# Kernel optimization log

Hardware: AMD Instinct MI355X
Metric: run time of the kernel (lower is better)

Reference implementation:

```python
import jax, jax.numpy as jnp
import numpy as np

LN_EPS = 1e-5
LEAKY_SLOPE = 0.01  # torch nn.LeakyReLU default negative_slope


def layer_norm(x, gamma, beta):
    mu = jnp.mean(x, axis=-1, keepdims=True)
    var = jnp.mean(jnp.square(x - mu), axis=-1, keepdims=True)
    return (x - mu) * jax.lax.rsqrt(var + LN_EPS) * gamma + beta


def setup_inputs() -> dict:
    key = jax.random.key(0)
    k1, k2, k3 = jax.random.split(key, 3)
    B, N, D = 32, 128, 64
    embeddings = jax.random.normal(k1, (B, N, D), dtype=jnp.float32)
    ln_gamma = jnp.ones((D,), dtype=jnp.float32)
    ln_beta = jnp.zeros((D,), dtype=jnp.float32)
    # nn.Linear(3*D, 1): weight [1, 3D], bias [1]
    bound = 1.0 / np.sqrt(3 * D)
    att_w = jax.random.uniform(k2, (1, 3 * D), dtype=jnp.float32, minval=-bound, maxval=bound)
    att_b = jax.random.uniform(k3, (1,), dtype=jnp.float32, minval=-bound, maxval=bound)
    return {"embeddings": embeddings, "ln_gamma": ln_gamma, "ln_beta": ln_beta,
            "att_w": att_w, "att_b": att_b}


def reference(embeddings, ln_gamma, ln_beta, att_w, att_b):
    # embeddings: [B, N, D]
    D = embeddings.shape[-1]
    w = att_w[0]
    w_q, w_k, w_v = w[:D], w[D:2 * D], w[2 * D:]

    # value = query * key (all-pairs elementwise product), [B, N, N, D]
    value = embeddings[:, :, None, :] * embeddings[:, None, :, :]

    # LayerNorm of the broadcast query/key is just a per-node LayerNorm,
    # broadcast N-fold -> compute once per node, then contract with the
    # corresponding slice of the concat-linear weight.
    ln_e = layer_norm(embeddings, ln_gamma, ln_beta)           # [B, N, D]
    q_score = ln_e @ w_q                                        # [B, N]
    k_score = ln_e @ w_k                                        # [B, N]
    v_score = jnp.einsum('bijd,d->bij', layer_norm(value, ln_gamma, ln_beta), w_v)

    # score = Linear(concat(wq, wk, wv)) : [B, N, N]
    score = q_score[:, :, None] + k_score[:, None, :] + v_score + att_b[0]
    score = jnp.where(score >= 0, score, LEAKY_SLOPE * score)   # LeakyReLU
    # dropout is identity in eval mode
    alphas = jax.nn.softmax(score, axis=-1)[..., None]          # [B, N, N, 1]
    return (alphas, value)
```

## Files before the change

### kernel.cpp

```cpp
#include <hip/hip_runtime.h>

#define N_TOK 128
#define DIM   64
#define LN_EPS 1e-5f
#define SLOPE  0.01f

__device__ __forceinline__ float wave_reduce_sum(float v) {
#pragma unroll
    for (int off = 32; off >= 1; off >>= 1) v += __shfl_xor(v, off, 64);
    return v;
}
__device__ __forceinline__ float wave_reduce_max(float v) {
#pragma unroll
    for (int off = 32; off >= 1; off >>= 1) v = fmaxf(v, __shfl_xor(v, off, 64));
    return v;
}

__global__ __launch_bounds__(256) void k0_row_stats(
        const float* __restrict__ emb, const float* __restrict__ gamma,
        const float* __restrict__ beta, const float* __restrict__ attw,
        float* __restrict__ q_ws, float* __restrict__ k_ws, int nrows) {
    int wave = threadIdx.x >> 6, lane = threadIdx.x & 63;
    int r = blockIdx.x * 4 + wave;
    if (r >= nrows) return;
    float e  = emb[r * DIM + lane];
    float g  = gamma[lane], bt = beta[lane];
    float wq = attw[lane], wk = attw[DIM + lane];
    float gwq = g * wq, gwk = g * wk;

    float se  = wave_reduce_sum(e);
    float se2 = wave_reduce_sum(e * e);
    float sq  = wave_reduce_sum(e * gwq);
    float sk  = wave_reduce_sum(e * gwk);
    float Sgq = wave_reduce_sum(gwq);
    float Sbq = wave_reduce_sum(bt * wq);
    float Sgk = wave_reduce_sum(gwk);
    float Sbk = wave_reduce_sum(bt * wk);

    if (lane == 0) {
        float mu  = se * (1.f / 64.f);
        float var = se2 * (1.f / 64.f) - mu * mu;
        float rsq = rsqrtf(var + LN_EPS);
        q_ws[r] = rsq * (sq - mu * Sgq) + Sbq;
        k_ws[r] = rsq * (sk - mu * Sgk) + Sbk;
    }
}

__global__ __launch_bounds__(256) void k1_scores(
        const float* __restrict__ emb, const float* __restrict__ gamma,
        const float* __restrict__ beta, const float* __restrict__ attw,
        const float* __restrict__ attb, const float* __restrict__ q_ws,
        const float* __restrict__ k_ws, float* __restrict__ alphas) {
    __shared__ float e_tr[DIM * N_TOK];
    __shared__ float EV[2][DIM];
    __shared__ float sc_lds[2][N_TOK];
    __shared__ float S[3];

    int b  = blockIdx.x >> 6;
    int i0 = (blockIdx.x & 63) * 2;

    const float4* E4 = (const float4*)(emb + (size_t)b * (N_TOK * DIM));
#pragma unroll
    for (int l = 0; l < 8; ++l) {
        int idx4 = l * 256 + threadIdx.x;
        int j = idx4 >> 4, c = idx4 & 15;
        float4 v = E4[idx4];
        int d0 = c * 4;
        e_tr[(d0 + 0) * N_TOK + (j ^ ((d0 + 0) & 31))] = v.x;
        e_tr[(d0 + 1) * N_TOK + (j ^ ((d0 + 1) & 31))] = v.y;
        e_tr[(d0 + 2) * N_TOK + (j ^ ((d0 + 2) & 31))] = v.z;
        e_tr[(d0 + 3) * N_TOK + (j ^ ((d0 + 3) & 31))] = v.w;
    }
    __syncthreads();

    if (threadIdx.x < 64) {
        int d = threadIdx.x;
        float g = gamma[d], bt = beta[d], wv = attw[2 * DIM + d];
        float sg = wave_reduce_sum(g * wv);
        float sb = wave_reduce_sum(bt * wv);
        if (d == 0) { S[0] = sg; S[1] = sb; S[2] = attb[0]; }
    } else if (threadIdx.x >= 128) {
        int t2 = threadIdx.x - 128;
        int il = t2 >> 6, d = t2 & 63;
        int i = i0 + il;
        float ei = e_tr[d * N_TOK + (i ^ (d & 31))];
        EV[il][d] = ei * gamma[d] * attw[2 * DIM + d];
    }
    __syncthreads();

    int w = threadIdx.x >> 6, lane = threadIdx.x & 63;
    int il = w >> 1, i = i0 + il;
    int j  = ((w & 1) << 6) | lane;
    float qi = q_ws[b * N_TOK + i];
    float kj = k_ws[b * N_TOK + j];
    float s1 = 0.f, s2 = 0.f, s3 = 0.f;
#pragma unroll
    for (int d = 0; d < DIM; ++d) {
        float ej = e_tr[d * N_TOK + (j ^ (d & 31))];
        float pi = e_tr[d * N_TOK + (i ^ (d & 31))];
        float t  = pi * ej;
        s1 += t;
        s2 = fmaf(t, t, s2);
        s3 = fmaf(EV[il][d], ej, s3);
    }
    float mu  = s1 * (1.f / 64.f);
    float var = s2 * (1.f / 64.f) - mu * mu;
    float rsq = rsqrtf(var + LN_EPS);
    float vsc = rsq * (s3 - mu * S[0]) + S[1];
    float sc  = qi + kj + vsc + S[2];
    sc = sc >= 0.f ? sc : SLOPE * sc;
    sc_lds[il][j] = sc;
    __syncthreads();

    if (w < 2) {
        float a  = sc_lds[w][lane];
        float bb = sc_lds[w][lane + 64];
        float m  = wave_reduce_max(fmaxf(a, bb));
        float ea = __expf(a - m), eb = __expf(bb - m);
        float s  = wave_reduce_sum(ea + eb);
        float inv = 1.f / s;
        float* arow = alphas + ((size_t)(b * N_TOK + i0 + w)) * N_TOK;
        arow[lane]      = ea * inv;
        arow[lane + 64] = eb * inv;
    }
}

__global__ __launch_bounds__(256) void k2_value(
        const float* __restrict__ emb, float4* __restrict__ out4, int total4) {
    const float4* E4 = (const float4*)emb;
    int tid = blockIdx.x * 256 + threadIdx.x;
    int stride = gridDim.x * 256;
    for (int idx4 = tid; idx4 < total4; idx4 += stride) {
        int c = idx4 & 15;
        int j = (idx4 >> 4) & 127;
        int i = (idx4 >> 11) & 127;
        int b = idx4 >> 18;
        float4 a = E4[(((b << 7) | i) << 4) | c];
        float4 e = E4[(((b << 7) | j) << 4) | c];
        float4 v;
        v.x = a.x * e.x; v.y = a.y * e.y; v.z = a.z * e.z; v.w = a.w * e.w;
        out4[idx4] = v;
    }
}

extern "C" void kernel_launch(void* const* d_in, const int* in_sizes, int n_in,
                              void* d_out, int out_size, void* d_ws, size_t ws_size,
                              hipStream_t stream) {
    const float* emb   = (const float*)d_in[0];
    const float* gamma = (const float*)d_in[1];
    const float* beta  = (const float*)d_in[2];
    const float* attw  = (const float*)d_in[3];
    const float* attb  = (const float*)d_in[4];
    float* out = (float*)d_out;

    int B = in_sizes[0] / (N_TOK * DIM);
    int nrows = B * N_TOK;
    float* q_ws = (float*)d_ws;
    float* k_ws = q_ws + nrows;

    float* alphas = out;
    float* value  = out + (size_t)nrows * N_TOK;
    int total4 = B * N_TOK * N_TOK * (DIM / 4);

    k0_row_stats<<<dim3((nrows + 3) / 4), dim3(256), 0, stream>>>(
        emb, gamma, beta, attw, q_ws, k_ws, nrows);
    k1_scores<<<dim3(B * 64), dim3(256), 0, stream>>>(
        emb, gamma, beta, attw, attb, q_ws, k_ws, alphas);
    k2_value<<<dim3(B * 128), dim3(256), 0, stream>>>(
        emb, (float4*)value, total4);
}
```

Before: 162.0 us.

## Fuse score computation and value product into one per-row kernel

Merges the score/softmax kernel and the value-writing kernel into one kernel with one block per (batch, query row). Each thread computes a float4 of the elementwise product, writes it to the value output, and reduces LayerNorm statistics across 16-lane groups with shuffles, so the products are computed once instead of twice. This drops the LDS transpose and one launch. In exchange it adds shuffle reductions per element group and rereads the embeddings from global or cache for every row.

```diff
diff --git a/kernel.cpp b/kernel.cpp
--- a/kernel.cpp
+++ b/kernel.cpp
@@ -46,100 +46,78 @@
     }
 }
 
-__global__ __launch_bounds__(256) void k1_scores(
+__global__ __launch_bounds__(256) void k12_fused(
         const float* __restrict__ emb, const float* __restrict__ gamma,
         const float* __restrict__ beta, const float* __restrict__ attw,
         const float* __restrict__ attb, const float* __restrict__ q_ws,
-        const float* __restrict__ k_ws, float* __restrict__ alphas) {
-    __shared__ float e_tr[DIM * N_TOK];
-    __shared__ float EV[2][DIM];
-    __shared__ float sc_lds[2][N_TOK];
-    __shared__ float S[3];
+        const float* __restrict__ k_ws, float* __restrict__ alphas,
+        float4* __restrict__ value4) {
+    __shared__ float sc_lds[N_TOK];
 
-    int b  = blockIdx.x >> 6;
-    int i0 = (blockIdx.x & 63) * 2;
+    int b = blockIdx.x >> 7;
+    int i = blockIdx.x & 127;
+    int c  = threadIdx.x & 15;
+    int jg = threadIdx.x >> 4;
 
-    const float4* E4 = (const float4*)(emb + (size_t)b * (N_TOK * DIM));
+    const float4* E4 = (const float4*)emb + ((size_t)(b * N_TOK) << 4);
+    float4 a4  = E4[(i << 4) | c];
+    float4 g4  = ((const float4*)gamma)[c];
+    float4 bt4 = ((const float4*)beta)[c];
+    float4 wv4 = ((const float4*)(attw + 2 * DIM))[c];
+    float gwx = g4.x * wv4.x, gwy = g4.y * wv4.y,
+          gwz = g4.z * wv4.z, gww = g4.w * wv4.w;
+
+    float Sg = gwx + gwy + gwz + gww;
+    float Sb = bt4.x * wv4.x + bt4.y * wv4.y + bt4.z * wv4.z + bt4.w * wv4.w;
 #pragma unroll
-    for (int l = 0; l < 8; ++l) {
-        int idx4 = l * 256 + threadIdx.x;
-        int j = idx4 >> 4, c = idx4 & 15;
-        float4 v = E4[idx4];
-        int d0 = c * 4;
-        e_tr[(d0 + 0) * N_TOK + (j ^ ((d0 + 0) & 31))] = v.x;
-        e_tr[(d0 + 1) * N_TOK + (j ^ ((d0 + 1) & 31))] = v.y;
-        e_tr[(d0 + 2) * N_TOK + (j ^ ((d0 + 2) & 31))] = v.z;
-        e_tr[(d0 + 3) * N_TOK + (j ^ ((d0 + 3) & 31))] = v.w;
+    for (int off = 1; off < 16; off <<= 1) {
+        Sg += __shfl_xor(Sg, off);
+        Sb += __shfl_xor(Sb, off);
+    }
+    float qi = q_ws[b * N_TOK + i] + attb[0];
+
+    float4* vrow = value4 + ((size_t)blockIdx.x << 11);
+
+#pragma unroll
+    for (int it = 0; it < 8; ++it) {
+        int j = (it << 4) | jg;
+        float4 e4 = E4[(j << 4) | c];
+        float4 t4;
+        t4.x = a4.x * e4.x; t4.y = a4.y * e4.y;
+        t4.z = a4.z * e4.z; t4.w = a4.w * e4.w;
+        vrow[(j << 4) | c] = t4;
+
+        float s1 = t4.x + t4.y + t4.z + t4.w;
+        float s2 = t4.x * t4.x + t4.y * t4.y + t4.z * t4.z + t4.w * t4.w;
+        float s3 = t4.x * gwx + t4.y * gwy + t4.z * gwz + t4.w * gww;
+#pragma unroll
+        for (int off = 1; off < 16; off <<= 1) {
+            s1 += __shfl_xor(s1, off);
+            s2 += __shfl_xor(s2, off);
+            s3 += __shfl_xor(s3, off);
+        }
+        if (c == 0) {
+            float mu  = s1 * (1.f / 64.f);
+            float var = s2 * (1.f / 64.f) - mu * mu;
+            float rsq = rsqrtf(var + LN_EPS);
+            float vsc = rsq * (s3 - mu * Sg) + Sb;
+            float sc  = qi + k_ws[b * N_TOK + j] + vsc;
+            sc_lds[j] = sc >= 0.f ? sc : SLOPE * sc;
+        }
     }
     __syncthreads();
 
     if (threadIdx.x < 64) {
-        int d = threadIdx.x;
-        float g = gamma[d], bt = beta[d], wv = attw[2 * DIM + d];
-        float sg = wave_reduce_sum(g * wv);
-        float sb = wave_reduce_sum(bt * wv);
-        if (d == 0) { S[0] = sg; S[1] = sb; S[2] = attb[0]; }
-    } else if (threadIdx.x >= 128) {
-        int t2 = threadIdx.x - 128;
-        int il = t2 >> 6, d = t2 & 63;
-        int i = i0 + il;
-        float ei = e_tr[d * N_TOK + (i ^ (d & 31))];
-        EV[il][d] = ei * gamma[d] * attw[2 * DIM + d];
-    }
-    __syncthreads();
-
-    int w = threadIdx.x >> 6, lane = threadIdx.x & 63;
-    int il = w >> 1, i = i0 + il;
-    int j  = ((w & 1) << 6) | lane;
-    float qi = q_ws[b * N_TOK + i];
-    float kj = k_ws[b * N_TOK + j];
-    float s1 = 0.f, s2 = 0.f, s3 = 0.f;
-#pragma unroll
-    for (int d = 0; d < DIM; ++d) {
-        float ej = e_tr[d * N_TOK + (j ^ (d & 31))];
-        float pi = e_tr[d * N_TOK + (i ^ (d & 31))];
-        float t  = pi * ej;
-        s1 += t;
-        s2 = fmaf(t, t, s2);
-        s3 = fmaf(EV[il][d], ej, s3);
-    }
-    float mu  = s1 * (1.f / 64.f);
-    float var = s2 * (1.f / 64.f) - mu * mu;
-    float rsq = rsqrtf(var + LN_EPS);
-    float vsc = rsq * (s3 - mu * S[0]) + S[1];
-    float sc  = qi + kj + vsc + S[2];
-    sc = sc >= 0.f ? sc : SLOPE * sc;
-    sc_lds[il][j] = sc;
-    __syncthreads();
-
-    if (w < 2) {
-        float a  = sc_lds[w][lane];
-        float bb = sc_lds[w][lane + 64];
-        float m  = wave_reduce_max(fmaxf(a, bb));
-        float ea = __expf(a - m), eb = __expf(bb - m);
+        int lane = threadIdx.x;
+        float va = sc_lds[lane];
+        float vb = sc_lds[lane + 64];
+        float m  = wave_reduce_max(fmaxf(va, vb));
+        float ea = __expf(va - m), eb = __expf(vb - m);
         float s  = wave_reduce_sum(ea + eb);
         float inv = 1.f / s;
-        float* arow = alphas + ((size_t)(b * N_TOK + i0 + w)) * N_TOK;
+        float* arow = alphas + ((size_t)blockIdx.x << 7);
         arow[lane]      = ea * inv;
         arow[lane + 64] = eb * inv;
-    }
-}
-
-__global__ __launch_bounds__(256) void k2_value(
-        const float* __restrict__ emb, float4* __restrict__ out4, int total4) {
-    const float4* E4 = (const float4*)emb;
-    int tid = blockIdx.x * 256 + threadIdx.x;
-    int stride = gridDim.x * 256;
-    for (int idx4 = tid; idx4 < total4; idx4 += stride) {
-        int c = idx4 & 15;
-        int j = (idx4 >> 4) & 127;
-        int i = (idx4 >> 11) & 127;
-        int b = idx4 >> 18;
-        float4 a = E4[(((b << 7) | i) << 4) | c];
-        float4 e = E4[(((b << 7) | j) << 4) | c];
-        float4 v;
-        v.x = a.x * e.x; v.y = a.y * e.y; v.z = a.z * e.z; v.w = a.w * e.w;
-        out4[idx4] = v;
     }
 }
 
@@ -160,12 +138,9 @@
 
     float* alphas = out;
     float* value  = out + (size_t)nrows * N_TOK;
-    int total4 = B * N_TOK * N_TOK * (DIM / 4);
 
     k0_row_stats<<<dim3((nrows + 3) / 4), dim3(256), 0, stream>>>(
         emb, gamma, beta, attw, q_ws, k_ws, nrows);
-    k1_scores<<<dim3(B * 64), dim3(256), 0, stream>>>(
-        emb, gamma, beta, attw, attb, q_ws, k_ws, alphas);
-    k2_value<<<dim3(B * 128), dim3(256), 0, stream>>>(
-        emb, (float4*)value, total4);
+    k12_fused<<<dim3(nrows), dim3(256), 0, stream>>>(
+        emb, gamma, beta, attw, attb, q_ws, k_ws, alphas, (float4*)value);
 }
```

Measured after the change: 151.3 us. 1.07x faster.
